# Kernel optimization log

Hardware: AMD Instinct MI355X
Metric: run time of the kernel (lower is better)

The kernel has to match this reference:

```python
import jax, jax.numpy as jnp
import numpy as np

B = 2048
L = 32000  # num_labels
E = 4      # number of experts


def setup_inputs() -> dict:
    key = jax.random.key(0)
    ks = jax.random.split(key, 5)
    labels = jax.random.randint(ks[0], (B,), 0, L)
    logits = [jax.random.normal(ks[i + 1], (B, L), dtype=jnp.float32) for i in range(E)]
    return {
        "labels": labels,
        "logits0": logits[0],
        "logits1": logits[1],
        "logits2": logits[2],
        "logits3": logits[3],
    }


def reference(labels, logits0, logits1, logits2, logits3):
    # stacked: (B, L, E)
    stacked = jnp.stack([logits0, logits1, logits2, logits3], axis=2)
    # per-expert predictions: (B, E)
    predictions = jnp.argmax(stacked, axis=1)
    correct = predictions == labels[:, None]  # (B, E) bool
    any_correct = jnp.any(correct, axis=1)  # (B,)
    # first correct expert index (argmax of bool returns first True)
    first_correct = jnp.argmax(correct, axis=1)  # (B,)
    # logits at the true label for each expert: (B, E)
    label_logits = jnp.take_along_axis(stacked, labels[:, None, None], axis=1)[:, 0, :]
    conf_best = jnp.argmax(label_logits, axis=1)  # (B,)
    best_expert = jnp.where(any_correct, first_correct, conf_best)  # (B,)
    # gather the chosen expert's logits: (B, L)
    effective = jnp.take_along_axis(stacked, best_expert[:, None, None], axis=2)[:, :, 0]
    return effective
```

## Files before the change

kernel.cpp:

```cpp
#include <hip/hip_runtime.h>

#define ROW_L 32000
#define NTHREADS 256

__global__ __launch_bounds__(NTHREADS) void oracle_best_expert_kernel(
    const int* __restrict__ labels,
    const float* __restrict__ g0,
    const float* __restrict__ g1,
    const float* __restrict__ g2,
    const float* __restrict__ g3,
    float* __restrict__ out)
{
    const int b = blockIdx.x;
    const size_t row = (size_t)b * ROW_L;
    const float* ptrs[4] = { g0 + row, g1 + row, g2 + row, g3 + row };

    const int tid = threadIdx.x;

    float vmax[4];
    int   vidx[4];
#pragma unroll
    for (int e = 0; e < 4; ++e) { vmax[e] = -__builtin_inff(); vidx[e] = 0; }

    const int NV = ROW_L / 4;
    for (int i = tid; i < NV; i += NTHREADS) {
        const int base = i * 4;
#pragma unroll
        for (int e = 0; e < 4; ++e) {
            const float4 v = reinterpret_cast<const float4*>(ptrs[e])[i];
            if (v.x > vmax[e]) { vmax[e] = v.x; vidx[e] = base + 0; }
            if (v.y > vmax[e]) { vmax[e] = v.y; vidx[e] = base + 1; }
            if (v.z > vmax[e]) { vmax[e] = v.z; vidx[e] = base + 2; }
            if (v.w > vmax[e]) { vmax[e] = v.w; vidx[e] = base + 3; }
        }
    }

#pragma unroll
    for (int off = 32; off >= 1; off >>= 1) {
#pragma unroll
        for (int e = 0; e < 4; ++e) {
            const float ov = __shfl_down(vmax[e], off, 64);
            const int   oi = __shfl_down(vidx[e], off, 64);
            if (ov > vmax[e] || (ov == vmax[e] && oi < vidx[e])) {
                vmax[e] = ov; vidx[e] = oi;
            }
        }
    }

    __shared__ float s_max[4][4];
    __shared__ int   s_idx[4][4];
    __shared__ int   s_best;
    const int wave = tid >> 6;
    const int lane = tid & 63;
    if (lane == 0) {
#pragma unroll
        for (int e = 0; e < 4; ++e) { s_max[wave][e] = vmax[e]; s_idx[wave][e] = vidx[e]; }
    }
    __syncthreads();

    if (tid == 0) {
        const int lab = labels[b];
        int best = -1;
#pragma unroll
        for (int e = 0; e < 4; ++e) {
            float m  = s_max[0][e];
            int   ix = s_idx[0][e];
#pragma unroll
            for (int w = 1; w < 4; ++w) {
                const float ov = s_max[w][e];
                const int   oi = s_idx[w][e];
                if (ov > m || (ov == m && oi < ix)) { m = ov; ix = oi; }
            }
            if (ix == lab && best < 0) best = e;
        }
        if (best < 0) {
            float bm = ptrs[0][lab];
            best = 0;
#pragma unroll
            for (int e = 1; e < 4; ++e) {
                const float v = ptrs[e][lab];
                if (v > bm) { bm = v; best = e; }
            }
        }
        s_best = best;
    }
    __syncthreads();

    const float* __restrict__ src = ptrs[s_best];
    float* __restrict__ dst = out + row;
    for (int i = tid; i < NV; i += NTHREADS) {
        reinterpret_cast<float4*>(dst)[i] = reinterpret_cast<const float4*>(src)[i];
    }
}

extern "C" void kernel_launch(void* const* d_in, const int* in_sizes, int n_in,
                              void* d_out, int out_size, void* d_ws, size_t ws_size,
                              hipStream_t stream) {
    const int*   labels = (const int*)d_in[0];
    const float* g0     = (const float*)d_in[1];
    const float* g1     = (const float*)d_in[2];
    const float* g2     = (const float*)d_in[3];
    const float* g3     = (const float*)d_in[4];
    float*       out    = (float*)d_out;

    const int B = in_sizes[0];
    oracle_best_expert_kernel<<<B, NTHREADS, 0, stream>>>(labels, g0, g1, g2, g3, out);
}
```

Baseline: 320.3 us.

## Assign one wave per expert for argmax, unroll loads, nontemporal output stores

Restructures the per-row argmax so each of the four waves scans one expert's row, instead of every thread scanning all four experts. This cuts the shuffle reduction to a single expert per wave and lets the cross-wave merge become a simple label check. The scan loop is unrolled 8-deep to put more independent loads in flight. The label logits are captured early into shared memory, and the copy phase uses an 8-deep unrolled load batch with nontemporal stores. Each wave now streams a whole row alone, which may change DRAM access patterns and per-wave latency balance.

```diff
diff --git a/kernel.cpp b/kernel.cpp
--- a/kernel.cpp
+++ b/kernel.cpp
@@ -1,9 +1,13 @@
 #include <hip/hip_runtime.h>
 
 #define ROW_L 32000
-#define NTHREADS 256
+#define NT    256
+#define NV    (ROW_L / 4)
+#define UF    8
 
-__global__ __launch_bounds__(NTHREADS) void oracle_best_expert_kernel(
+typedef float f32x4 __attribute__((ext_vector_type(4)));
+
+__global__ __launch_bounds__(NT) void oracle_best_expert_kernel(
     const int* __restrict__ labels,
     const float* __restrict__ g0,
     const float* __restrict__ g1,
@@ -13,83 +17,103 @@
 {
     const int b = blockIdx.x;
     const size_t row = (size_t)b * ROW_L;
-    const float* ptrs[4] = { g0 + row, g1 + row, g2 + row, g3 + row };
+    const float* __restrict__ p0 = g0 + row;
+    const float* __restrict__ p1 = g1 + row;
+    const float* __restrict__ p2 = g2 + row;
+    const float* __restrict__ p3 = g3 + row;
 
-    const int tid = threadIdx.x;
+    const int tid  = threadIdx.x;
+    const int wave = tid >> 6;
+    const int lane = tid & 63;
 
-    float vmax[4];
-    int   vidx[4];
+    __shared__ float s_labv[4];
+    __shared__ float s_max[4];
+    __shared__ int   s_idx[4];
+    __shared__ int   s_best;
+
+    const float* __restrict__ pw = (wave == 0) ? p0 :
+                                   (wave == 1) ? p1 :
+                                   (wave == 2) ? p2 : p3;
+    const f32x4* __restrict__ q = (const f32x4*)pw;
+
+    const int lab = labels[b];
+    if (lane == 0) s_labv[wave] = pw[lab];
+
+    float m  = -__builtin_inff();
+    int   mi = 0;
+
+#pragma unroll 1
+    for (int it = 0; it < 15; ++it) {
+        const int base = it * (UF * 64) + lane;
+        f32x4 v[UF];
 #pragma unroll
-    for (int e = 0; e < 4; ++e) { vmax[e] = -__builtin_inff(); vidx[e] = 0; }
-
-    const int NV = ROW_L / 4;
-    for (int i = tid; i < NV; i += NTHREADS) {
-        const int base = i * 4;
+        for (int u = 0; u < UF; ++u) v[u] = q[base + u * 64];
 #pragma unroll
-        for (int e = 0; e < 4; ++e) {
-            const float4 v = reinterpret_cast<const float4*>(ptrs[e])[i];
-            if (v.x > vmax[e]) { vmax[e] = v.x; vidx[e] = base + 0; }
-            if (v.y > vmax[e]) { vmax[e] = v.y; vidx[e] = base + 1; }
-            if (v.z > vmax[e]) { vmax[e] = v.z; vidx[e] = base + 2; }
-            if (v.w > vmax[e]) { vmax[e] = v.w; vidx[e] = base + 3; }
+        for (int u = 0; u < UF; ++u) {
+            const int bi = (base + u * 64) * 4;
+            if (v[u].x > m) { m = v[u].x; mi = bi + 0; }
+            if (v[u].y > m) { m = v[u].y; mi = bi + 1; }
+            if (v[u].z > m) { m = v[u].z; mi = bi + 2; }
+            if (v[u].w > m) { m = v[u].w; mi = bi + 3; }
+        }
+    }
+    {
+        const int base = 15 * (UF * 64) + lane;
+        f32x4 v[5];
+#pragma unroll
+        for (int u = 0; u < 5; ++u) v[u] = q[base + u * 64];
+#pragma unroll
+        for (int u = 0; u < 5; ++u) {
+            const int bi = (base + u * 64) * 4;
+            if (v[u].x > m) { m = v[u].x; mi = bi + 0; }
+            if (v[u].y > m) { m = v[u].y; mi = bi + 1; }
+            if (v[u].z > m) { m = v[u].z; mi = bi + 2; }
+            if (v[u].w > m) { m = v[u].w; mi = bi + 3; }
         }
     }
 
 #pragma unroll
     for (int off = 32; off >= 1; off >>= 1) {
-#pragma unroll
-        for (int e = 0; e < 4; ++e) {
-            const float ov = __shfl_down(vmax[e], off, 64);
-            const int   oi = __shfl_down(vidx[e], off, 64);
-            if (ov > vmax[e] || (ov == vmax[e] && oi < vidx[e])) {
-                vmax[e] = ov; vidx[e] = oi;
-            }
-        }
+        const float ov = __shfl_down(m, off, 64);
+        const int   oi = __shfl_down(mi, off, 64);
+        if (ov > m || (ov == m && oi < mi)) { m = ov; mi = oi; }
     }
-
-    __shared__ float s_max[4][4];
-    __shared__ int   s_idx[4][4];
-    __shared__ int   s_best;
-    const int wave = tid >> 6;
-    const int lane = tid & 63;
-    if (lane == 0) {
-#pragma unroll
-        for (int e = 0; e < 4; ++e) { s_max[wave][e] = vmax[e]; s_idx[wave][e] = vidx[e]; }
-    }
+    if (lane == 0) { s_max[wave] = m; s_idx[wave] = mi; }
     __syncthreads();
 
     if (tid == 0) {
-        const int lab = labels[b];
         int best = -1;
 #pragma unroll
-        for (int e = 0; e < 4; ++e) {
-            float m  = s_max[0][e];
-            int   ix = s_idx[0][e];
+        for (int e = 0; e < 4; ++e)
+            if (best < 0 && s_idx[e] == lab) best = e;
+        if (best < 0) {
+            float bm = s_labv[0]; best = 0;
 #pragma unroll
-            for (int w = 1; w < 4; ++w) {
-                const float ov = s_max[w][e];
-                const int   oi = s_idx[w][e];
-                if (ov > m || (ov == m && oi < ix)) { m = ov; ix = oi; }
-            }
-            if (ix == lab && best < 0) best = e;
-        }
-        if (best < 0) {
-            float bm = ptrs[0][lab];
-            best = 0;
-#pragma unroll
-            for (int e = 1; e < 4; ++e) {
-                const float v = ptrs[e][lab];
-                if (v > bm) { bm = v; best = e; }
-            }
+            for (int e = 1; e < 4; ++e)
+                if (s_labv[e] > bm) { bm = s_labv[e]; best = e; }
         }
         s_best = best;
     }
     __syncthreads();
 
-    const float* __restrict__ src = ptrs[s_best];
-    float* __restrict__ dst = out + row;
-    for (int i = tid; i < NV; i += NTHREADS) {
-        reinterpret_cast<float4*>(dst)[i] = reinterpret_cast<const float4*>(src)[i];
+    const int be = s_best;
+    const f32x4* __restrict__ src = (const f32x4*)((be == 0) ? p0 :
+                                                   (be == 1) ? p1 :
+                                                   (be == 2) ? p2 : p3);
+    f32x4* __restrict__ dst = (f32x4*)(out + row);
+#pragma unroll 1
+    for (int i0 = tid; i0 < NV; i0 += NT * UF) {
+        f32x4 t[UF];
+#pragma unroll
+        for (int u = 0; u < UF; ++u) {
+            const int i = i0 + u * NT;
+            if (i < NV) t[u] = src[i];
+        }
+#pragma unroll
+        for (int u = 0; u < UF; ++u) {
+            const int i = i0 + u * NT;
+            if (i < NV) __builtin_nontemporal_store(t[u], &dst[i]);
+        }
     }
 }
 
@@ -104,5 +128,5 @@
     float*       out    = (float*)d_out;
 
     const int B = in_sizes[0];
-    oracle_best_expert_kernel<<<B, NTHREADS, 0, stream>>>(labels, g0, g1, g2, g3, out);
+    oracle_best_expert_kernel<<<B, NT, 0, stream>>>(labels, g0, g1, g2, g3, out);
 }
```

Result: faster. 267.7 us (-16.4%).
